# Kernel tuning notes

Hardware: AMD Instinct MI355X
Metric: run time of the kernel (lower is better)

## Reference

```python
import jax, jax.numpy as jnp
import numpy as np

B, S, D = 2, 2048, 2048
H, KV, HD = 32, 8, 64
REP = H // KV  # 4


def setup_inputs() -> dict:
    key = jax.random.key(0)
    ks = jax.random.split(key, 5)
    x = jax.random.normal(ks[0], (B, S, D), jnp.float32)
    # Llama rope frequencies: theta=10000, pairs of adjacent dims
    inv_freq = 1.0 / (10000.0 ** (np.arange(0, HD, 2, dtype=np.float64) / HD))  # [HD/2]
    ang = np.outer(np.arange(S, dtype=np.float64), inv_freq)  # [S, HD/2]
    freqs_cis = jnp.asarray(np.stack([np.cos(ang), np.sin(ang)], axis=-1), jnp.float32)  # [S, HD/2, 2]
    wq = jax.random.normal(ks[1], (H * HD, D), jnp.float32) * 0.02
    wk = jax.random.normal(ks[2], (KV * HD, D), jnp.float32) * 0.02
    wv = jax.random.normal(ks[3], (KV * HD, D), jnp.float32) * 0.02
    wo = jax.random.normal(ks[4], (D, H * HD), jnp.float32) * 0.02
    return {"x": x, "freqs_cis": freqs_cis, "wq": wq, "wk": wk, "wv": wv, "wo": wo}


def _apply_rope(t, cos, sin):
    # t: [B,S,nh,HD]; cos/sin: [S,HD/2]; complex multiply on adjacent pairs
    b, s, nh, hd = t.shape
    t2 = t.reshape(b, s, nh, hd // 2, 2)
    tr, ti = t2[..., 0], t2[..., 1]
    c = cos[None, :, None, :]
    sn = sin[None, :, None, :]
    out = jnp.stack([tr * c - ti * sn, tr * sn + ti * c], axis=-1)
    return out.reshape(b, s, nh, hd)


def reference(x, freqs_cis, wq, wk, wv, wo):
    # QKV projections (torch Linear: y = x @ W.T)
    q = jnp.einsum('bsd,ed->bse', x, wq).reshape(B, S, H, HD)
    k = jnp.einsum('bsd,ed->bse', x, wk).reshape(B, S, KV, HD)
    v = jnp.einsum('bsd,ed->bse', x, wv).reshape(B, S, KV, HD)
    cos, sin = freqs_cis[..., 0], freqs_cis[..., 1]
    q = _apply_rope(q, cos, sin)
    k = _apply_rope(k, cos, sin)
    # GQA without materializing repeated K/V: group query heads by KV head
    qg = q.reshape(B, S, KV, REP, HD)
    scale = 1.0 / jnp.sqrt(jnp.asarray(HD, q.dtype))
    scores = jnp.einsum('bsgrd,btgd->bgrst', qg, k) * scale  # [B,KV,REP,S,S]
    causal = jnp.tril(jnp.ones((S, S), bool))
    scores = jnp.where(causal, scores, -jnp.inf)
    p = jax.nn.softmax(scores, axis=-1)
    o = jnp.einsum('bgrst,btgd->bsgrd', p, v).reshape(B, S, H * HD)
    return jnp.einsum('bse,de->bsd', o, wo)
```

## Files before the change

kernel.cpp:

```cpp
#include <hip/hip_runtime.h>
#include <cstdint>
#include <cstddef>

#define B_ 2
#define S_ 2048
#define D_ 2048
#define H_ 32
#define KV_ 8
#define HD_ 64
#define M_ (B_*S_)
#define EQ_ (H_*HD_)
#define EK_ (KV_*HD_)

typedef unsigned short u16;
typedef __attribute__((ext_vector_type(8))) short s16x8;
typedef __attribute__((ext_vector_type(4))) float f32x4;

#define QSCALE 0.18033688011112042f
#define EXPOFF 15.869645449778564f

#if __has_builtin(__builtin_amdgcn_exp2f)
#define EXP2(x) __builtin_amdgcn_exp2f(x)
#else
#define EXP2(x) __expf((x) * 0.6931471805599453f)
#endif

__device__ __forceinline__ u16 f2bf(float f) {
  unsigned u = __float_as_uint(f);
  u += 0x7fffu + ((u >> 16) & 1u);
  return (u16)(u >> 16);
}
__device__ __forceinline__ unsigned pk2(float a, float b) {
  unsigned ua = __float_as_uint(a) + 0x8000u;
  unsigned ub = __float_as_uint(b) + 0x8000u;
  return __builtin_amdgcn_perm(ub, ua, 0x07060302);
}
__device__ __forceinline__ f32x4 mfma16(s16x8 a, s16x8 b, f32x4 c) {
  return __builtin_amdgcn_mfma_f32_16x16x32_bf16(a, b, c, 0, 0, 0);
}
__device__ __forceinline__ void gl_lds16(const void* g, void* l) {
  __builtin_amdgcn_global_load_lds(
      (const __attribute__((address_space(1))) void*)g,
      (__attribute__((address_space(3))) void*)l, 16, 0, 0);
}

__global__ void cast_all(const float4* __restrict__ x, const float4* __restrict__ wq,
                         const float4* __restrict__ wk, const float4* __restrict__ wv,
                         const float4* __restrict__ wo, ushort4* __restrict__ dst) {
  int i = blockIdx.x * 256 + threadIdx.x;
  const float4* src; int off;
  if (i < 2097152)      { src = x;  off = i; }
  else if (i < 3145728) { src = wq; off = i - 2097152; }
  else if (i < 3407872) { src = wk; off = i - 3145728; }
  else if (i < 3670016) { src = wv; off = i - 3407872; }
  else                  { src = wo; off = i - 3670016; }
  float4 v = src[off];
  ushort4 r;
  r.x = f2bf(v.x); r.y = f2bf(v.y); r.z = f2bf(v.z); r.w = f2bf(v.w);
  dst[i] = r;
}

__global__ __launch_bounds__(256)
void gemm_qkv(const u16* __restrict__ A, const u16* __restrict__ Bw,
              u16* __restrict__ qb, u16* __restrict__ kb, u16* __restrict__ vtb,
              const float* __restrict__ fc) {
  __shared__ __align__(16) u16 As[2][128 * 32];
  __shared__ __align__(16) u16 Bs[2][96 * 32];
  const int tid  = threadIdx.x;
  const int lane = tid & 63;
  const int wave = tid >> 6;
  const int m0 = blockIdx.y * 128;
  const int n0 = blockIdx.x * 96;
  const int wm = (wave >> 1) * 64;
  const int wn = (wave & 1) * 48;
  const int l15 = lane & 15;
  const int quad = lane >> 4;

  const int ca0 = tid,      ra0 = ca0 >> 2, pa0 = ca0 & 3;
  const int ca1 = tid + 256, ra1 = ca1 >> 2, pa1 = ca1 & 3;
  const int cb0 = tid,      rb0 = cb0 >> 2, pb0 = cb0 & 3;
  const int cb1 = tid + 256, rb1 = cb1 >> 2, pb1 = cb1 & 3;
  const u16* Ap0 = A + (size_t)(m0 + ra0) * D_ + (pa0 ^ ((ra0 >> 1) & 3)) * 8;
  const u16* Ap1 = A + (size_t)(m0 + ra1) * D_ + (pa1 ^ ((ra1 >> 1) & 3)) * 8;
  const u16* Bp0 = Bw + (size_t)(n0 + rb0) * D_ + (pb0 ^ ((rb0 >> 1) & 3)) * 8;
  const u16* Bp1 = Bw + (size_t)(n0 + rb1) * D_ + (pb1 ^ ((rb1 >> 1) & 3)) * 8;
  const bool doB1 = (tid < 128);

  f32x4 acc[4][3] = {};

  gl_lds16(Ap0, &As[0][ca0 * 8]);
  gl_lds16(Ap1, &As[0][ca1 * 8]);
  gl_lds16(Bp0, &Bs[0][cb0 * 8]);
  if (doB1) gl_lds16(Bp1, &Bs[0][cb1 * 8]);
  __syncthreads();

  for (int ks = 0; ks < 64; ++ks) {
    if (ks + 1 < 64) {
      const int nb = (ks + 1) & 1;
      const int ko = (ks + 1) * 32;
      gl_lds16(Ap0 + ko, &As[nb][ca0 * 8]);
      gl_lds16(Ap1 + ko, &As[nb][ca1 * 8]);
      gl_lds16(Bp0 + ko, &Bs[nb][cb0 * 8]);
      if (doB1) gl_lds16(Bp1 + ko, &Bs[nb][cb1 * 8]);
    }

    const u16* as = &As[ks & 1][0];
    const u16* bs = &Bs[ks & 1][0];
    s16x8 af[4], bfr[3];
    #pragma unroll
    for (int mi = 0; mi < 4; ++mi) {
      int row = wm + mi * 16 + l15;
      af[mi] = *(const s16x8*)&as[row * 32 + (quad ^ ((row >> 1) & 3)) * 8];
    }
    #pragma unroll
    for (int ni = 0; ni < 3; ++ni) {
      int row = wn + ni * 16 + l15;
      bfr[ni] = *(const s16x8*)&bs[row * 32 + (quad ^ ((row >> 1) & 3)) * 8];
    }
    #pragma unroll
    for (int mi = 0; mi < 4; ++mi)
      #pragma unroll
      for (int ni = 0; ni < 3; ++ni)
        acc[mi][ni] = mfma16(af[mi], bfr[ni], acc[mi][ni]);

    __syncthreads();
  }

  const float sg = (l15 & 1) ? 1.f : -1.f;
  #pragma unroll
  for (int mi = 0; mi < 4; ++mi) {
    #pragma unroll
    for (int ni = 0; ni < 3; ++ni) {
      const int col = n0 + wn + ni * 16 + l15;
      if (col < 2560) {
        const bool isQ = (col < 2048);
        u16* dst = isQ ? qb : kb;
        const int ncol0 = isQ ? 0 : 2048;
        const int ndim  = isQ ? EQ_ : EK_;
        const float scale = isQ ? QSCALE : 1.0f;
        const int ip = (col & 63) >> 1;
        #pragma unroll
        for (int r = 0; r < 4; ++r) {
          int row = m0 + wm + mi * 16 + quad * 4 + r;
          const float* fr = fc + (size_t)(row & (S_ - 1)) * 64;
          float c  = fr[ip * 2];
          float sn = fr[ip * 2 + 1];
          float v = acc[mi][ni][r];
          float p = __shfl_xor(v, 1, 64);
          float o = (v * c + sg * (p * sn)) * scale;
          dst[(size_t)row * ndim + col - ncol0] = f2bf(o);
        }
      } else {
        const int vcol = col - 2560;
        uint2 w;
        w.x = pk2(acc[mi][ni][0], acc[mi][ni][1]);
        w.y = pk2(acc[mi][ni][2], acc[mi][ni][3]);
        *(uint2*)(vtb + (size_t)vcol * M_ + m0 + wm + mi * 16 + quad * 4) = w;
      }
    }
  }
}

__global__ __launch_bounds__(256)
void gemm_o(const u16* __restrict__ A, const u16* __restrict__ Bw, float* __restrict__ C,
            int Ndim, int Kdim) {
  __shared__ __align__(16) u16 As[2][64 * 32];
  __shared__ __align__(16) u16 Bs[2][128 * 32];
  const int tid  = threadIdx.x;
  const int lane = tid & 63;
  const int wave = tid >> 6;
  const int m0 = blockIdx.y * 64;
  const int n0 = blockIdx.x * 128;
  const int wm = (wave >> 1) * 32;
  const int wn = (wave & 1) * 64;
  const int l15 = lane & 15;
  const int quad = lane >> 4;

  const int ca0 = tid,      ra0 = ca0 >> 2, pa0 = ca0 & 3;
  const int cb0 = tid,      rb0 = cb0 >> 2, pb0 = cb0 & 3;
  const int cb1 = tid + 256, rb1 = cb1 >> 2, pb1 = cb1 & 3;
  const u16* Ap0 = A + (size_t)(m0 + ra0) * Kdim + (pa0 ^ ((ra0 >> 1) & 3)) * 8;
  const u16* Bp0 = Bw + (size_t)(n0 + rb0) * Kdim + (pb0 ^ ((rb0 >> 1) & 3)) * 8;
  const u16* Bp1 = Bw + (size_t)(n0 + rb1) * Kdim + (pb1 ^ ((rb1 >> 1) & 3)) * 8;

  f32x4 acc[2][4] = {};

  const int nsteps = Kdim >> 5;

  gl_lds16(Ap0, &As[0][ca0 * 8]);
  gl_lds16(Bp0, &Bs[0][cb0 * 8]);
  gl_lds16(Bp1, &Bs[0][cb1 * 8]);
  __syncthreads();

  for (int ks = 0; ks < nsteps; ++ks) {
    if (ks + 1 < nsteps) {
      const int nb = (ks + 1) & 1;
      const int ko = (ks + 1) * 32;
      gl_lds16(Ap0 + ko, &As[nb][ca0 * 8]);
      gl_lds16(Bp0 + ko, &Bs[nb][cb0 * 8]);
      gl_lds16(Bp1 + ko, &Bs[nb][cb1 * 8]);
    }

    const u16* as = &As[ks & 1][0];
    const u16* bs = &Bs[ks & 1][0];
    s16x8 af[2], bfr[4];
    #pragma unroll
    for (int mi = 0; mi < 2; ++mi) {
      int row = wm + mi * 16 + l15;
      af[mi] = *(const s16x8*)&as[row * 32 + (quad ^ ((row >> 1) & 3)) * 8];
    }
    #pragma unroll
    for (int ni = 0; ni < 4; ++ni) {
      int row = wn + ni * 16 + l15;
      bfr[ni] = *(const s16x8*)&bs[row * 32 + (quad ^ ((row >> 1) & 3)) * 8];
    }
    #pragma unroll
    for (int mi = 0; mi < 2; ++mi)
      #pragma unroll
      for (int ni = 0; ni < 4; ++ni)
        acc[mi][ni] = mfma16(af[mi], bfr[ni], acc[mi][ni]);

    __syncthreads();
  }

  #pragma unroll
  for (int mi = 0; mi < 2; ++mi) {
    #pragma unroll
    for (int r = 0; r < 4; ++r) {
      int row = m0 + wm + mi * 16 + quad * 4 + r;
      size_t base = (size_t)row * Ndim + n0 + wn;
      #pragma unroll
      for (int ni = 0; ni < 4; ++ni)
        C[base + ni * 16 + l15] = acc[mi][ni][r];
    }
  }
}

__global__ __launch_bounds__(256, 4)
void flash_attn(const u16* __restrict__ qb, const u16* __restrict__ kb,
                const u16* __restrict__ vtb, u16* __restrict__ ob) {
  const int bx = blockIdx.x;
  const int h  = blockIdx.y;
  const int b  = blockIdx.z;
  const int g  = h >> 2;
  const int tid  = threadIdx.x;
  const int lane = tid & 63;
  const int wave = tid >> 6;
  const int l15  = lane & 15;
  const int quad = lane >> 4;
  const int kq   = quad * 8;

  const int Tlo = bx, Thi = 31 - bx;
  const int n_lo = Tlo + 1, n_hi = Thi + 1;
  const int rL = Tlo * 64 + wave * 16;
  const int rH = Thi * 64 + wave * 16;
  const int rowL = rL + l15;
  const int rowH = rH + l15;

  __shared__ __align__(16) u16 Ks[2][8 * 512];
  __shared__ __align__(16) u16 Vs[2][8 * 512];

  const u16* qpL = qb + (size_t)(b * S_ + rL + l15) * EQ_ + h * HD_;
  const u16* qpH = qb + (size_t)(b * S_ + rH + l15) * EQ_ + h * HD_;
  s16x8 qL0 = *(const s16x8*)(qpL + kq);
  s16x8 qL1 = *(const s16x8*)(qpL + 32 + kq);
  s16x8 qH0 = *(const s16x8*)(qpH + kq);
  s16x8 qH1 = *(const s16x8*)(qpH + 32 + kq);

  f32x4 OL[4] = {}, OH[4] = {};
  float sumL = 0.f, sumH = 0.f;

  const int sw = wave & 1;
  const bool doK = (wave < 2);

  const int tl = (lane & 0x23) | ((lane & 0x0C) << 1) | ((lane & 0x10) >> 2);

  const u16* stbase;
  size_t     tstride;
  if (doK) {
    stbase  = kb + (size_t)(b * S_ + tl) * EK_ + g * HD_ + sw * 32;
    tstride = (size_t)64 * EK_;
  } else {
    stbase  = vtb + (size_t)(g * HD_ + lane) * M_ + b * S_ + sw * 32;
    tstride = 64;
  }
  const int ldoff = sw * 4 * 512 + lane * 8;
  u16* mybuf0 = (doK ? &Ks[0][0] : &Vs[0][0]) + ldoff;
  u16* mybuf1 = (doK ? &Ks[1][0] : &Vs[1][0]) + ldoff;

  #pragma unroll
  for (int r = 0; r < 4; ++r)
    gl_lds16(stbase + r * 8, mybuf0 + r * 512);
  __syncthreads();

  union PU { s16x8 v; unsigned u[4]; };

  for (int kt = 0; kt < n_hi; ++kt) {
    const int t0 = kt * 64;
    const u16* kcur = &Ks[kt & 1][0];
    const u16* vcur = &Vs[kt & 1][0];

    if (kt + 1 < n_hi) {
      const u16* src = stbase + (size_t)(kt + 1) * tstride;
      u16* dst = ((kt + 1) & 1) ? mybuf1 : mybuf0;
      #pragma unroll
      for (int r = 0; r < 4; ++r)
        gl_lds16(src + r * 8, dst + r * 512);
    }

    const bool do_lo = (kt < n_lo);
    const bool mH = (kt == n_hi - 1);
    const bool mL = (kt == n_lo - 1);

    s16x8 kk0[4], kk1[4];
    #pragma unroll
    for (int ts = 0; ts < 4; ++ts) {
      kk0[ts] = *(const s16x8*)&kcur[quad * 512 + (ts * 16 + l15) * 8];
      kk1[ts] = *(const s16x8*)&kcur[(4 + quad) * 512 + (ts * 16 + l15) * 8];
    }

    PU pH0u, pH1u;
    {
      f32x4 sH[4];
      #pragma unroll
      for (int ts = 0; ts < 4; ++ts) {
        f32x4 s = {};
        s = mfma16(kk0[ts], qH0, s);
        s = mfma16(kk1[ts], qH1, s);
        sH[ts] = s;
      }
      if (mH) {
        #pragma unroll
        for (int ts = 0; ts < 4; ++ts) {
          const int tb = t0 + ((ts & 2) << 4) + ((ts & 1) << 2) + quad * 8;
          #pragma unroll
          for (int r = 0; r < 4; ++r) if (tb + r > rowH) sH[ts][r] = -1e30f;
        }
      }
      float e[16];
      #pragma unroll
      for (int ts = 0; ts < 4; ++ts)
        #pragma unroll
        for (int r = 0; r < 4; ++r) {
          float x = EXP2(sH[ts][r] - EXPOFF);
          e[ts * 4 + r] = x;
          sumH += x;
        }
      pH0u.u[0] = pk2(e[0],  e[1]);  pH0u.u[1] = pk2(e[2],  e[3]);
      pH0u.u[2] = pk2(e[4],  e[5]);  pH0u.u[3] = pk2(e[6],  e[7]);
      pH1u.u[0] = pk2(e[8],  e[9]);  pH1u.u[1] = pk2(e[10], e[11]);
      pH1u.u[2] = pk2(e[12], e[13]); pH1u.u[3] = pk2(e[14], e[15]);
    }

    PU pL0u, pL1u;
    pL0u.v = s16x8{}; pL1u.v = s16x8{};
    if (do_lo) {
      f32x4 sL[4];
      #pragma unroll
      for (int ts = 0; ts < 4; ++ts) {
        f32x4 s = {};
        s = mfma16(kk0[ts], qL0, s);
        s = mfma16(kk1[ts], qL1, s);
        sL[ts] = s;
      }
      if (mL) {
        #pragma unroll
        for (int ts = 0; ts < 4; ++ts) {
          const int tb = t0 + ((ts & 2) << 4) + ((ts & 1) << 2) + quad * 8;
          #pragma unroll
          for (int r = 0; r < 4; ++r) if (tb + r > rowL) sL[ts][r] = -1e30f;
        }
      }
      float e[16];
      #pragma unroll
      for (int ts = 0; ts < 4; ++ts)
        #pragma unroll
        for (int r = 0; r < 4; ++r) {
          float x = EXP2(sL[ts][r] - EXPOFF);
          e[ts * 4 + r] = x;
          sumL += x;
        }
      pL0u.u[0] = pk2(e[0],  e[1]);  pL0u.u[1] = pk2(e[2],  e[3]);
      pL0u.u[2] = pk2(e[4],  e[5]);  pL0u.u[3] = pk2(e[6],  e[7]);
      pL1u.u[0] = pk2(e[8],  e[9]);  pL1u.u[1] = pk2(e[10], e[11]);
      pL1u.u[2] = pk2(e[12], e[13]); pL1u.u[3] = pk2(e[14], e[15]);
    }

    #pragma unroll
    for (int df = 0; df < 4; ++df) {
      s16x8 v0 = *(const s16x8*)&vcur[quad * 512 + (df * 16 + l15) * 8];
      s16x8 v1 = *(const s16x8*)&vcur[(4 + quad) * 512 + (df * 16 + l15) * 8];
      OH[df] = mfma16(v1, pH1u.v, mfma16(v0, pH0u.v, OH[df]));
      if (do_lo) OL[df] = mfma16(v1, pL1u.v, mfma16(v0, pL0u.v, OL[df]));
    }

    __syncthreads();
  }

  sumH += __shfl_xor(sumH, 16, 64); sumH += __shfl_xor(sumH, 32, 64);
  sumL += __shfl_xor(sumL, 16, 64); sumL += __shfl_xor(sumL, 32, 64);
  float invH = 1.f / sumH, invL = 1.f / sumL;

  {
    u16* op = ob + (size_t)(b * S_ + rowH) * EQ_ + h * HD_;
    #pragma unroll
    for (int df = 0; df < 4; ++df) {
      uint2 w;
      w.x = pk2(OH[df][0] * invH, OH[df][1] * invH);
      w.y = pk2(OH[df][2] * invH, OH[df][3] * invH);
      *(uint2*)(op + df * 16 + quad * 4) = w;
    }
  }
  {
    u16* op = ob + (size_t)(b * S_ + rowL) * EQ_ + h * HD_;
    #pragma unroll
    for (int df = 0; df < 4; ++df) {
      uint2 w;
      w.x = pk2(OL[df][0] * invL, OL[df][1] * invL);
      w.y = pk2(OL[df][2] * invL, OL[df][3] * invL);
      *(uint2*)(op + df * 16 + quad * 4) = w;
    }
  }
}

extern "C" void kernel_launch(void* const* d_in, const int* in_sizes, int n_in,
                              void* d_out, int out_size, void* d_ws, size_t ws_size,
                              hipStream_t stream) {
  (void)in_sizes; (void)n_in; (void)out_size; (void)ws_size;
  const float* x  = (const float*)d_in[0];
  const float* fc = (const float*)d_in[1];
  const float* wq = (const float*)d_in[2];
  const float* wk = (const float*)d_in[3];
  const float* wv = (const float*)d_in[4];
  const float* wo = (const float*)d_in[5];
  float* out = (float*)d_out;
  char* ws = (char*)d_ws;

  u16* xb  = (u16*)(ws);
  u16* wqb = (u16*)(ws + 16777216);
  u16* wob = (u16*)(ws + 29360128);
  u16* qb  = (u16*)(ws + 37748736);
  u16* kb  = (u16*)(ws + 54525952);
  u16* vtb = (u16*)(ws + 58720256);
  u16* ob  = (u16*)(ws + 62914560);

  cast_all<<<18432, 256, 0, stream>>>((const float4*)x, (const float4*)wq,
                                      (const float4*)wk, (const float4*)wv,
                                      (const float4*)wo, (ushort4*)ws);

  gemm_qkv<<<dim3(32, 32), 256, 0, stream>>>(xb, wqb, qb, kb, vtb, fc);

  flash_attn<<<dim3(16, 32, 2), 256, 0, stream>>>(qb, kb, vtb, ob);

  gemm_o<<<dim3(16, 64), 256, 0, stream>>>(ob, wob, out, D_, EQ_);
}
```

Measured before the change: 317.2 us.

## Triple-buffer GEMM LDS pipelines and widen QKV tile to 128x128

Both projection GEMMs move from double to triple-buffered LDS staging, prefetching two K-steps ahead. A partial vmcnt wait plus a raw barrier replaces the full __syncthreads, so global loads can stay in flight across iterations. The QKV GEMM tile grows from 128x96 to 128x128, which cuts the grid from 32x32 to 24x32 and gives more MFMA work per block. In exchange the kernels use more LDS and registers, which may lower occupancy.

```diff
diff --git a/kernel.cpp b/kernel.cpp
--- a/kernel.cpp
+++ b/kernel.cpp
@@ -64,73 +64,75 @@
 void gemm_qkv(const u16* __restrict__ A, const u16* __restrict__ Bw,
               u16* __restrict__ qb, u16* __restrict__ kb, u16* __restrict__ vtb,
               const float* __restrict__ fc) {
-  __shared__ __align__(16) u16 As[2][128 * 32];
-  __shared__ __align__(16) u16 Bs[2][96 * 32];
+  __shared__ __align__(16) u16 As[3][128 * 32];
+  __shared__ __align__(16) u16 Bs[3][128 * 32];
   const int tid  = threadIdx.x;
   const int lane = tid & 63;
   const int wave = tid >> 6;
   const int m0 = blockIdx.y * 128;
-  const int n0 = blockIdx.x * 96;
+  const int n0 = blockIdx.x * 128;
   const int wm = (wave >> 1) * 64;
-  const int wn = (wave & 1) * 48;
+  const int wn = (wave & 1) * 64;
   const int l15 = lane & 15;
   const int quad = lane >> 4;
 
-  const int ca0 = tid,      ra0 = ca0 >> 2, pa0 = ca0 & 3;
+  const int ca0 = tid,       ra0 = ca0 >> 2, pa0 = ca0 & 3;
   const int ca1 = tid + 256, ra1 = ca1 >> 2, pa1 = ca1 & 3;
-  const int cb0 = tid,      rb0 = cb0 >> 2, pb0 = cb0 & 3;
-  const int cb1 = tid + 256, rb1 = cb1 >> 2, pb1 = cb1 & 3;
   const u16* Ap0 = A + (size_t)(m0 + ra0) * D_ + (pa0 ^ ((ra0 >> 1) & 3)) * 8;
   const u16* Ap1 = A + (size_t)(m0 + ra1) * D_ + (pa1 ^ ((ra1 >> 1) & 3)) * 8;
-  const u16* Bp0 = Bw + (size_t)(n0 + rb0) * D_ + (pb0 ^ ((rb0 >> 1) & 3)) * 8;
-  const u16* Bp1 = Bw + (size_t)(n0 + rb1) * D_ + (pb1 ^ ((rb1 >> 1) & 3)) * 8;
-  const bool doB1 = (tid < 128);
-
-  f32x4 acc[4][3] = {};
-
-  gl_lds16(Ap0, &As[0][ca0 * 8]);
-  gl_lds16(Ap1, &As[0][ca1 * 8]);
-  gl_lds16(Bp0, &Bs[0][cb0 * 8]);
-  if (doB1) gl_lds16(Bp1, &Bs[0][cb1 * 8]);
-  __syncthreads();
+  const u16* Bp0 = Bw + (size_t)(n0 + ra0) * D_ + (pa0 ^ ((ra0 >> 1) & 3)) * 8;
+  const u16* Bp1 = Bw + (size_t)(n0 + ra1) * D_ + (pa1 ^ ((ra1 >> 1) & 3)) * 8;
+
+  f32x4 acc[4][4] = {};
+
+  u16 *a0 = &As[0][0], *a1 = &As[1][0], *a2 = &As[2][0];
+  u16 *b0 = &Bs[0][0], *b1 = &Bs[1][0], *b2 = &Bs[2][0];
+
+  gl_lds16(Ap0, a0 + ca0 * 8);  gl_lds16(Ap1, a0 + ca1 * 8);
+  gl_lds16(Bp0, b0 + ca0 * 8);  gl_lds16(Bp1, b0 + ca1 * 8);
+  gl_lds16(Ap0 + 32, a1 + ca0 * 8);  gl_lds16(Ap1 + 32, a1 + ca1 * 8);
+  gl_lds16(Bp0 + 32, b1 + ca0 * 8);  gl_lds16(Bp1 + 32, b1 + ca1 * 8);
+  asm volatile("s_waitcnt vmcnt(4)" ::: "memory");
+  __builtin_amdgcn_s_barrier();
 
   for (int ks = 0; ks < 64; ++ks) {
-    if (ks + 1 < 64) {
-      const int nb = (ks + 1) & 1;
-      const int ko = (ks + 1) * 32;
-      gl_lds16(Ap0 + ko, &As[nb][ca0 * 8]);
-      gl_lds16(Ap1 + ko, &As[nb][ca1 * 8]);
-      gl_lds16(Bp0 + ko, &Bs[nb][cb0 * 8]);
-      if (doB1) gl_lds16(Bp1 + ko, &Bs[nb][cb1 * 8]);
-    }
-
-    const u16* as = &As[ks & 1][0];
-    const u16* bs = &Bs[ks & 1][0];
-    s16x8 af[4], bfr[3];
+    if (ks < 62) {
+      const int ko = (ks + 2) * 32;
+      gl_lds16(Ap0 + ko, a2 + ca0 * 8);  gl_lds16(Ap1 + ko, a2 + ca1 * 8);
+      gl_lds16(Bp0 + ko, b2 + ca0 * 8);  gl_lds16(Bp1 + ko, b2 + ca1 * 8);
+    }
+
+    s16x8 af[4], bfr[4];
     #pragma unroll
     for (int mi = 0; mi < 4; ++mi) {
       int row = wm + mi * 16 + l15;
-      af[mi] = *(const s16x8*)&as[row * 32 + (quad ^ ((row >> 1) & 3)) * 8];
-    }
-    #pragma unroll
-    for (int ni = 0; ni < 3; ++ni) {
+      af[mi] = *(const s16x8*)&a0[row * 32 + (quad ^ ((row >> 1) & 3)) * 8];
+    }
+    #pragma unroll
+    for (int ni = 0; ni < 4; ++ni) {
       int row = wn + ni * 16 + l15;
-      bfr[ni] = *(const s16x8*)&bs[row * 32 + (quad ^ ((row >> 1) & 3)) * 8];
+      bfr[ni] = *(const s16x8*)&b0[row * 32 + (quad ^ ((row >> 1) & 3)) * 8];
     }
     #pragma unroll
     for (int mi = 0; mi < 4; ++mi)
       #pragma unroll
-      for (int ni = 0; ni < 3; ++ni)
+      for (int ni = 0; ni < 4; ++ni)
         acc[mi][ni] = mfma16(af[mi], bfr[ni], acc[mi][ni]);
 
-    __syncthreads();
+    if (ks < 62) asm volatile("s_waitcnt vmcnt(4)" ::: "memory");
+    else         asm volatile("s_waitcnt vmcnt(0)" ::: "memory");
+    __builtin_amdgcn_s_barrier();
+
+    u16* t;
+    t = a0; a0 = a1; a1 = a2; a2 = t;
+    t = b0; b0 = b1; b1 = b2; b2 = t;
   }
 
   const float sg = (l15 & 1) ? 1.f : -1.f;
   #pragma unroll
   for (int mi = 0; mi < 4; ++mi) {
     #pragma unroll
-    for (int ni = 0; ni < 3; ++ni) {
+    for (int ni = 0; ni < 4; ++ni) {
       const int col = n0 + wn + ni * 16 + l15;
       if (col < 2560) {
         const bool isQ = (col < 2048);
@@ -164,8 +166,8 @@
 __global__ __launch_bounds__(256)
 void gemm_o(const u16* __restrict__ A, const u16* __restrict__ Bw, float* __restrict__ C,
             int Ndim, int Kdim) {
-  __shared__ __align__(16) u16 As[2][64 * 32];
-  __shared__ __align__(16) u16 Bs[2][128 * 32];
+  __shared__ __align__(16) u16 As[3][64 * 32];
+  __shared__ __align__(16) u16 Bs[3][128 * 32];
   const int tid  = threadIdx.x;
   const int lane = tid & 63;
   const int wave = tid >> 6;
@@ -176,43 +178,42 @@
   const int l15 = lane & 15;
   const int quad = lane >> 4;
 
-  const int ca0 = tid,      ra0 = ca0 >> 2, pa0 = ca0 & 3;
-  const int cb0 = tid,      rb0 = cb0 >> 2, pb0 = cb0 & 3;
+  const int ca0 = tid,       ra0 = ca0 >> 2, pa0 = ca0 & 3;
   const int cb1 = tid + 256, rb1 = cb1 >> 2, pb1 = cb1 & 3;
   const u16* Ap0 = A + (size_t)(m0 + ra0) * Kdim + (pa0 ^ ((ra0 >> 1) & 3)) * 8;
-  const u16* Bp0 = Bw + (size_t)(n0 + rb0) * Kdim + (pb0 ^ ((rb0 >> 1) & 3)) * 8;
+  const u16* Bp0 = Bw + (size_t)(n0 + ra0) * Kdim + (pa0 ^ ((ra0 >> 1) & 3)) * 8;
   const u16* Bp1 = Bw + (size_t)(n0 + rb1) * Kdim + (pb1 ^ ((rb1 >> 1) & 3)) * 8;
 
   f32x4 acc[2][4] = {};
-
   const int nsteps = Kdim >> 5;
 
-  gl_lds16(Ap0, &As[0][ca0 * 8]);
-  gl_lds16(Bp0, &Bs[0][cb0 * 8]);
-  gl_lds16(Bp1, &Bs[0][cb1 * 8]);
-  __syncthreads();
+  u16 *a0 = &As[0][0], *a1 = &As[1][0], *a2 = &As[2][0];
+  u16 *b0 = &Bs[0][0], *b1 = &Bs[1][0], *b2 = &Bs[2][0];
+
+  gl_lds16(Ap0, a0 + ca0 * 8);
+  gl_lds16(Bp0, b0 + ca0 * 8);  gl_lds16(Bp1, b0 + cb1 * 8);
+  gl_lds16(Ap0 + 32, a1 + ca0 * 8);
+  gl_lds16(Bp0 + 32, b1 + ca0 * 8);  gl_lds16(Bp1 + 32, b1 + cb1 * 8);
+  asm volatile("s_waitcnt vmcnt(3)" ::: "memory");
+  __builtin_amdgcn_s_barrier();
 
   for (int ks = 0; ks < nsteps; ++ks) {
-    if (ks + 1 < nsteps) {
-      const int nb = (ks + 1) & 1;
-      const int ko = (ks + 1) * 32;
-      gl_lds16(Ap0 + ko, &As[nb][ca0 * 8]);
-      gl_lds16(Bp0 + ko, &Bs[nb][cb0 * 8]);
-      gl_lds16(Bp1 + ko, &Bs[nb][cb1 * 8]);
-    }
-
-    const u16* as = &As[ks & 1][0];
-    const u16* bs = &Bs[ks & 1][0];
+    if (ks + 2 < nsteps) {
+      const int ko = (ks + 2) * 32;
+      gl_lds16(Ap0 + ko, a2 + ca0 * 8);
+      gl_lds16(Bp0 + ko, b2 + ca0 * 8);  gl_lds16(Bp1 + ko, b2 + cb1 * 8);
+    }
+
     s16x8 af[2], bfr[4];
     #pragma unroll
     for (int mi = 0; mi < 2; ++mi) {
       int row = wm + mi * 16 + l15;
-      af[mi] = *(const s16x8*)&as[row * 32 + (quad ^ ((row >> 1) & 3)) * 8];
+      af[mi] = *(const s16x8*)&a0[row * 32 + (quad ^ ((row >> 1) & 3)) * 8];
     }
     #pragma unroll
     for (int ni = 0; ni < 4; ++ni) {
       int row = wn + ni * 16 + l15;
-      bfr[ni] = *(const s16x8*)&bs[row * 32 + (quad ^ ((row >> 1) & 3)) * 8];
+      bfr[ni] = *(const s16x8*)&b0[row * 32 + (quad ^ ((row >> 1) & 3)) * 8];
     }
     #pragma unroll
     for (int mi = 0; mi < 2; ++mi)
@@ -220,7 +221,13 @@
       for (int ni = 0; ni < 4; ++ni)
         acc[mi][ni] = mfma16(af[mi], bfr[ni], acc[mi][ni]);
 
-    __syncthreads();
+    if (ks + 2 < nsteps) asm volatile("s_waitcnt vmcnt(3)" ::: "memory");
+    else                 asm volatile("s_waitcnt vmcnt(0)" ::: "memory");
+    __builtin_amdgcn_s_barrier();
+
+    u16* t;
+    t = a0; a0 = a1; a1 = a2; a2 = t;
+    t = b0; b0 = b1; b1 = b2; b2 = t;
   }
 
   #pragma unroll
@@ -448,7 +455,7 @@
                                       (const float4*)wk, (const float4*)wv,
                                       (const float4*)wo, (ushort4*)ws);
 
-  gemm_qkv<<<dim3(32, 32), 256, 0, stream>>>(xb, wqb, qb, kb, vtb, fc);
+  gemm_qkv<<<dim3(24, 32), 256, 0, stream>>>(xb, wqb, qb, kb, vtb, fc);
 
   flash_attn<<<dim3(16, 32, 2), 256, 0, stream>>>(qb, kb, vtb, ob);
 
```

Result: slower. 328.1 us (+3.4%).
